# Performance work log

Measured on AMD Instinct MI355X. Metric: run time of the kernel, lower is better.

## Reference

```python
import jax, jax.numpy as jnp
import numpy as np

A = 64    # number of discrete actions (expert matrices)
D = 512   # input/output feature dim
B = 2048  # batch size


def setup_inputs() -> dict:
    key = jax.random.key(0)
    kx, ka, kw, kb = jax.random.split(key, 4)
    stdv = 1.0 / np.sqrt(D)  # matches torch init: uniform(-stdv, stdv), stdv = 1/sqrt(weight.size(1))
    x = jax.random.normal(kx, (B, D), dtype=jnp.float32)
    a = jax.random.randint(ka, (B,), 0, A, dtype=jnp.int64)
    weight = jax.random.uniform(kw, (A, D, D), dtype=jnp.float32, minval=-stdv, maxval=stdv)
    bias = jax.random.uniform(kb, (A, D), dtype=jnp.float32, minval=-stdv, maxval=stdv)
    return {"x": x, "a": a, "weight": weight, "bias": bias}


def reference(x, a, weight, bias):
    # Per-sample weight gather + batched matvec:
    #   z[b, i] = sum_j weight[a[b], i, j] * x[b, j] + bias[a[b], i]
    w = weight[a]                              # [B, D, D] gathered per-sample matrices
    z = jnp.einsum('bij,bj->bi', w, x)         # batched matvec
    z = z + bias[a]                            # per-sample bias gather + add
    return z
```

## Files before the change

### kernel.cpp

```cpp
#include <hip/hip_runtime.h>


#define NA 64
#define DD 512
#define NB 2048
#define BN 64
#define NW 4
#define MT 48
#define BK 32
#define NSTEPS 16
#define NSLOT 3

typedef __bf16  bf16x8  __attribute__((ext_vector_type(8)));
typedef __bf16  bf16x4  __attribute__((ext_vector_type(4)));
typedef float   floatx4 __attribute__((ext_vector_type(4)));

#define GLD16(g, l)                                                         \
  __builtin_amdgcn_global_load_lds(                                         \
      (const __attribute__((address_space(1))) void*)(g),                   \
      (__attribute__((address_space(3))) void*)(l), 16, 0, 0)
#define VMCNT(n) asm volatile("s_waitcnt vmcnt(" #n ")" ::: "memory")
#define LGKMCNT0 asm volatile("s_waitcnt lgkmcnt(0)" ::: "memory")
#define SBAR     __builtin_amdgcn_s_barrier()
#define SCHED0   __builtin_amdgcn_sched_barrier(0)

static __device__ inline bf16x8 cvt8(floatx4 lo, floatx4 hi) {
    bf16x8 r;
    r[0] = (__bf16)lo[0]; r[1] = (__bf16)lo[1];
    r[2] = (__bf16)lo[2]; r[3] = (__bf16)lo[3];
    r[4] = (__bf16)hi[0]; r[5] = (__bf16)hi[1];
    r[6] = (__bf16)hi[2]; r[7] = (__bf16)hi[3];
    return r;
}

__global__ __launch_bounds__(256, 2) void dl_fused(
        const float* __restrict__ x,
        const int*   __restrict__ act,
        const float* __restrict__ weight,
        const float* __restrict__ bias,
        float*       __restrict__ out)
{
    const int a    = blockIdx.x;
    const int tid  = threadIdx.x;
    const int wave = tid >> 6;
    const int lane = tid & 63;
    const int l16  = lane & 15;
    const int kgrp = lane >> 4;
    const int h    = l16 & 7;
    const int colbase = blockIdx.y * BN;
    const int ncol    = colbase + wave * 16 + l16;

    __shared__ __align__(16) __bf16 Xs[MT][DD];
    __shared__ __align__(16) float  Wl[NSLOT][BN][BK];
    __shared__ unsigned short s_perm[NB];
    __shared__ int s_wcnt[NW];

    const float* wtile = weight + (size_t)a * DD * DD + (size_t)colbase * DD;

    const int r8 = lane >> 3;
    const int u8 = lane & 7;

    auto issue_step = [&](int slot, int s) {
#pragma unroll
        for (int c = 0; c < 2; ++c)
            GLD16(wtile + (size_t)(wave * 16 + c * 8 + r8) * DD + s * BK
                        + ((u8 ^ r8) << 2),
                  (char*)&Wl[slot][wave * 16 + c * 8][0]);
    };

    const int ibase = wave * (NB / NW);
    int myact[NB / NW / 64];
#pragma unroll
    for (int it = 0; it < NB / NW / 64; ++it)
        myact[it] = act[ibase + it * 64 + lane];

    issue_step(0, 0);
    issue_step(1, 1);
    issue_step(2, 2);

    int wcnt = 0;
#pragma unroll
    for (int it = 0; it < NB / NW / 64; ++it)
        wcnt += (int)__popcll(__ballot(myact[it] == a));
    if (lane == 0) s_wcnt[wave] = wcnt;
    LGKMCNT0; SBAR;
    int cnt = 0, off = 0;
#pragma unroll
    for (int v = 0; v < NW; ++v) {
        const int c = s_wcnt[v];
        if (v < wave) off += c;
        cnt += c;
    }
    if (cnt == 0) { VMCNT(0); return; }
#pragma unroll
    for (int it = 0; it < NB / NW / 64; ++it) {
        unsigned long long m = __ballot(myact[it] == a);
        if (myact[it] == a) {
            int pos = off + (int)__popcll(m & ((1ull << lane) - 1ull));
            s_perm[pos] = (unsigned short)(ibase + it * 64 + lane);
        }
        off += (int)__popcll(m);
    }
    LGKMCNT0; SBAR;

    const float bias_v = bias[(size_t)a * DD + ncol];
    const int   srow   = tid >> 5;
    const int   skk    = (tid & 31) << 2;

    for (int m0 = 0; m0 < cnt; m0 += MT) {
        if (m0 > 0) {
            issue_step(0, 0); issue_step(1, 1); issue_step(2, 2);
        }
        const int rem    = min(cnt - m0, MT);
        const int nchunk = (rem + 15) >> 4;

        floatx4 xv[24];
#pragma unroll
        for (int i = 0; i < 6; ++i) {
            const int r  = srow + 8 * i;
            const int rr = (r < rem) ? r : (rem - 1);
            const float* xr = x + (size_t)s_perm[m0 + rr] * DD;
#pragma unroll
            for (int j = 0; j < 4; ++j)
                xv[i * 4 + j] = *(const floatx4*)(xr + skk + 128 * j);
        }
#pragma unroll
        for (int i = 0; i < 6; ++i) {
            const int r = srow + 8 * i;
            if (r < rem) {
                const int rs = (r & 7) << 3;
#pragma unroll
                for (int j = 0; j < 4; ++j) {
                    const int f0 = skk + 128 * j;
                    bf16x4 bv;
#pragma unroll
                    for (int q = 0; q < 4; ++q) bv[q] = (__bf16)xv[i * 4 + j][q];
                    *(bf16x4*)&Xs[r][f0 ^ rs] = bv;
                }
            }
        }
        LGKMCNT0; SBAR;

        floatx4 acc[3] = {{0,0,0,0},{0,0,0,0},{0,0,0,0}};

        auto compute = [&](int slot, int s) {
            const char* wl = (const char*)&Wl[slot][wave * 16 + l16][0];
            const floatx4 blo = *(const floatx4*)(wl + (((2 * kgrp)     ^ h) << 4));
            const floatx4 bhi = *(const floatx4*)(wl + (((2 * kgrp + 1) ^ h) << 4));
            const bf16x8 bfrag = cvt8(blo, bhi);
            const int kb = (s * BK + kgrp * 8) ^ (h << 3);
#pragma unroll
            for (int mc = 0; mc < 3; ++mc) {
                if (mc < nchunk) {
                    const bf16x8 afrag = *(const bf16x8*)&Xs[mc * 16 + l16][kb];
                    acc[mc] = __builtin_amdgcn_mfma_f32_16x16x32_bf16(
                                  afrag, bfrag, acc[mc], 0, 0, 0);
                }
            }
        };

#pragma unroll
        for (int i = 0; i < NSTEPS; ++i) {
            if (i < NSTEPS - 2)       { VMCNT(4); }
            else if (i == NSTEPS - 2) { VMCNT(2); }
            else                      { VMCNT(0); }
            SCHED0;
            compute(i % NSLOT, i);
            if (i + NSLOT < NSTEPS) issue_step(i % NSLOT, i + NSLOT);
        }

#pragma unroll
        for (int mc = 0; mc < 3; ++mc) {
            if (mc < nchunk) {
#pragma unroll
                for (int r = 0; r < 4; ++r) {
                    const int mloc = mc * 16 + kgrp * 4 + r;
                    if (mloc < rem)
                        out[(size_t)s_perm[m0 + mloc] * DD + ncol] =
                            acc[mc][r] + bias_v;
                }
            }
        }
        LGKMCNT0; SBAR;
    }
}

extern "C" void kernel_launch(void* const* d_in, const int* in_sizes, int n_in,
                              void* d_out, int out_size, void* d_ws, size_t ws_size,
                              hipStream_t stream) {
    const float* x      = (const float*)d_in[0];
    const int*   act    = (const int*)  d_in[1];
    const float* weight = (const float*)d_in[2];
    const float* bias   = (const float*)d_in[3];
    float*       out    = (float*)d_out;

    dl_fused<<<dim3(NA, DD / BN), 256, 0, stream>>>(x, act, weight, bias, out);
}
```

Baseline: 18.88 us.

## Precompute action buckets in a separate kernel instead of per-block scans

Adds a single-block bucketing kernel that builds a histogram, prefix offsets and a permutation of batch indices by action into workspace. The GEMM kernel then reads its count and offset directly and loads the relevant slice of the permutation into shared memory, instead of every block scanning all 2048 actions. This removes redundant per-block scanning and ballot work, at the cost of an extra kernel launch and a serial dependency on a one-block kernel. The perm slice load covers 512 entries, which assumes no action has more than roughly 500 samples.

```diff
diff --git a/kernel.cpp b/kernel.cpp
--- a/kernel.cpp
+++ b/kernel.cpp
@@ -33,11 +33,56 @@
     return r;
 }
 
-__global__ __launch_bounds__(256, 2) void dl_fused(
+__global__ __launch_bounds__(256) void dl_bucket(const int* __restrict__ act,
+                                                 int* __restrict__ counts,
+                                                 int* __restrict__ offsets,
+                                                 unsigned short* __restrict__ perm) {
+    __shared__ int s_hist[4][NA];
+    __shared__ int s_cur[4][NA];
+    const int t = threadIdx.x;
+    const int w = t >> 6;
+    ((int*)s_hist)[t] = 0;
+    __syncthreads();
+    int myact[8];
+#pragma unroll
+    for (int i = 0; i < 8; ++i) {
+        myact[i] = act[t + i * 256];
+        atomicAdd(&s_hist[w][myact[i]], 1);
+    }
+    __syncthreads();
+    if (t < NA) {
+        const int h0 = s_hist[0][t], h1 = s_hist[1][t];
+        const int h2 = s_hist[2][t], h3 = s_hist[3][t];
+        const int tot = h0 + h1 + h2 + h3;
+        int incl = tot;
+#pragma unroll
+        for (int d = 1; d < 64; d <<= 1) {
+            int up = __shfl_up(incl, d, 64);
+            if (t >= d) incl += up;
+        }
+        const int excl = incl - tot;
+        counts[t]  = tot;
+        offsets[t] = excl;
+        s_cur[0][t] = excl;
+        s_cur[1][t] = excl + h0;
+        s_cur[2][t] = excl + h0 + h1;
+        s_cur[3][t] = excl + h0 + h1 + h2;
+    }
+    __syncthreads();
+#pragma unroll
+    for (int i = 0; i < 8; ++i) {
+        int pos = atomicAdd(&s_cur[w][myact[i]], 1);
+        perm[pos] = (unsigned short)(t + i * 256);
+    }
+}
+
+__global__ __launch_bounds__(256, 2) void dl_gemm(
         const float* __restrict__ x,
-        const int*   __restrict__ act,
         const float* __restrict__ weight,
         const float* __restrict__ bias,
+        const int*   __restrict__ counts,
+        const int*   __restrict__ offsets,
+        const unsigned short* __restrict__ perm,
         float*       __restrict__ out)
 {
     const int a    = blockIdx.x;
@@ -50,10 +95,13 @@
     const int colbase = blockIdx.y * BN;
     const int ncol    = colbase + wave * 16 + l16;
 
+    const int cnt = counts[a];
+    if (cnt == 0) return;
+    const int base = offsets[a];
+
     __shared__ __align__(16) __bf16 Xs[MT][DD];
     __shared__ __align__(16) float  Wl[NSLOT][BN][BK];
-    __shared__ unsigned short s_perm[NB];
-    __shared__ int s_wcnt[NW];
+    __shared__ __align__(16) unsigned short s_perm[512];
 
     const float* wtile = weight + (size_t)a * DD * DD + (size_t)colbase * DD;
 
@@ -68,58 +116,29 @@
                   (char*)&Wl[slot][wave * 16 + c * 8][0]);
     };
 
-    const int ibase = wave * (NB / NW);
-    int myact[NB / NW / 64];
-#pragma unroll
-    for (int it = 0; it < NB / NW / 64; ++it)
-        myact[it] = act[ibase + it * 64 + lane];
-
-    issue_step(0, 0);
-    issue_step(1, 1);
-    issue_step(2, 2);
-
-    int wcnt = 0;
-#pragma unroll
-    for (int it = 0; it < NB / NW / 64; ++it)
-        wcnt += (int)__popcll(__ballot(myact[it] == a));
-    if (lane == 0) s_wcnt[wave] = wcnt;
-    LGKMCNT0; SBAR;
-    int cnt = 0, off = 0;
-#pragma unroll
-    for (int v = 0; v < NW; ++v) {
-        const int c = s_wcnt[v];
-        if (v < wave) off += c;
-        cnt += c;
-    }
-    if (cnt == 0) { VMCNT(0); return; }
-#pragma unroll
-    for (int it = 0; it < NB / NW / 64; ++it) {
-        unsigned long long m = __ballot(myact[it] == a);
-        if (myact[it] == a) {
-            int pos = off + (int)__popcll(m & ((1ull << lane) - 1ull));
-            s_perm[pos] = (unsigned short)(ibase + it * 64 + lane);
-        }
-        off += (int)__popcll(m);
-    }
-    LGKMCNT0; SBAR;
-
     const float bias_v = bias[(size_t)a * DD + ncol];
     const int   srow   = tid >> 5;
     const int   skk    = (tid & 31) << 2;
 
     for (int m0 = 0; m0 < cnt; m0 += MT) {
-        if (m0 > 0) {
-            issue_step(0, 0); issue_step(1, 1); issue_step(2, 2);
-        }
         const int rem    = min(cnt - m0, MT);
         const int nchunk = (rem + 15) >> 4;
+
+        const int bm = base + m0;
+        const int b0 = min(bm & ~7, NB - 512);
+        const int d  = bm - b0;
+        GLD16((const char*)perm + 2 * b0 + lane * 16, (char*)s_perm);
+        issue_step(0, 0);
+        issue_step(1, 1);
+        issue_step(2, 2);
+        VMCNT(6);
 
         floatx4 xv[24];
 #pragma unroll
         for (int i = 0; i < 6; ++i) {
             const int r  = srow + 8 * i;
             const int rr = (r < rem) ? r : (rem - 1);
-            const float* xr = x + (size_t)s_perm[m0 + rr] * DD;
+            const float* xr = x + (size_t)(int)s_perm[d + rr] * DD;
 #pragma unroll
             for (int j = 0; j < 4; ++j)
                 xv[i * 4 + j] = *(const floatx4*)(xr + skk + 128 * j);
@@ -176,7 +195,7 @@
                 for (int r = 0; r < 4; ++r) {
                     const int mloc = mc * 16 + kgrp * 4 + r;
                     if (mloc < rem)
-                        out[(size_t)s_perm[m0 + mloc] * DD + ncol] =
+                        out[(size_t)(int)s_perm[d + mloc] * DD + ncol] =
                             acc[mc][r] + bias_v;
                 }
             }
@@ -194,5 +213,11 @@
     const float* bias   = (const float*)d_in[3];
     float*       out    = (float*)d_out;
 
-    dl_fused<<<dim3(NA, DD / BN), 256, 0, stream>>>(x, act, weight, bias, out);
-}
+    int*            counts  = (int*)d_ws;
+    int*            offsets = counts + NA;
+    unsigned short* perm    = (unsigned short*)(offsets + NA);
+
+    dl_bucket<<<1, 256, 0, stream>>>(act, counts, offsets, perm);
+    dl_gemm<<<dim3(NA, DD / BN), 256, 0, stream>>>(x, weight, bias,
+                                                   counts, offsets, perm, out);
+}
```

After: 23.88 us. +26.5%, slower.
